# Performance work log

Measured on AMD Instinct MI355X. Metric: run time of the kernel, lower is better.

## Reference

```python
import jax, jax.numpy as jnp
import numpy as np

N_EMBD = 1024
N_HEAD = 16
HEAD_DIM = N_EMBD // N_HEAD


def setup_inputs() -> dict:
    key = jax.random.key(0)
    ks = jax.random.split(key, 9)
    B, T, C = 4, 2048, N_EMBD
    s = 1.0 / np.sqrt(C)
    return {
        "x": jax.random.normal(ks[0], (B, T, C), dtype=jnp.float32),
        "Wq": jax.random.normal(ks[1], (C, C), dtype=jnp.float32) * s,
        "bq": jnp.zeros((C,), dtype=jnp.float32),
        "Wk": jax.random.normal(ks[2], (C, C), dtype=jnp.float32) * s,
        "bk": jnp.zeros((C,), dtype=jnp.float32),
        "Wv": jax.random.normal(ks[3], (C, C), dtype=jnp.float32) * s,
        "bv": jnp.zeros((C,), dtype=jnp.float32),
        "Wo": jax.random.normal(ks[4], (C, C), dtype=jnp.float32) * s,
        "bo": jnp.zeros((C,), dtype=jnp.float32),
    }


def reference(x, Wq, bq, Wk, bk, Wv, bv, Wo, bo):
    B, T, C = x.shape
    H, D = N_HEAD, HEAD_DIM
    # torch Linear: y = x @ W.T + b ; here W stored as (in, out) so y = x @ W + b
    q = (x @ Wq + bq).reshape(B, T, H, D).transpose(0, 2, 1, 3)  # [B,H,T,D]
    k = (x @ Wk + bk).reshape(B, T, H, D).transpose(0, 2, 1, 3)
    v = (x @ Wv + bv).reshape(B, T, H, D).transpose(0, 2, 1, 3)
    scores = jnp.einsum('bhqd,bhkd->bhqk', q, k) / jnp.sqrt(jnp.float32(D))
    causal = jnp.tril(jnp.ones((T, T), dtype=bool))  # [T,T]
    scores = jnp.where(causal[None, None, :, :], scores, -jnp.inf)
    weights = jax.nn.softmax(scores, axis=-1)
    # dropout disabled (eval mode / deterministic reference)
    out = jnp.einsum('bhqk,bhkd->bhqd', weights, v)  # [B,H,T,D]
    out = out.transpose(0, 2, 1, 3).reshape(B, T, C)
    return out @ Wo + bo
```

## Files before the change

### kernel.cpp

```cpp
#include <hip/hip_runtime.h>
#include <stdint.h>
#include <stddef.h>

#define NB 4
#define NT 2048
#define NC 1024
#define NH 16
#define ND 64
#define NM (NB*NT)

typedef __bf16 bf16_t;
typedef __attribute__((ext_vector_type(8)))  __bf16 bf16x8;
typedef __attribute__((ext_vector_type(4)))  __bf16 bf16x4;
typedef __attribute__((ext_vector_type(2)))  __bf16 bf16x2;
typedef __attribute__((ext_vector_type(4)))  float  f32x4;
typedef __attribute__((ext_vector_type(16))) float  f32x16;
typedef __attribute__((ext_vector_type(4)))  unsigned int u32x4;

#define QK_SCALE_LOG2E 0.18033688011112042f

__device__ __forceinline__ f32x4 mfma_bf16(bf16x8 a, bf16x8 b, f32x4 c) {
  return __builtin_amdgcn_mfma_f32_16x16x32_bf16(a, b, c, 0, 0, 0);
}
__device__ __forceinline__ f32x16 mfma32(bf16x8 a, bf16x8 b, f32x16 c) {
  return __builtin_amdgcn_mfma_f32_32x32x16_bf16(a, b, c, 0, 0, 0);
}

__device__ __forceinline__ void gld_lds16(const void* g, void* l) {
  __builtin_amdgcn_global_load_lds(
      (const __attribute__((address_space(1))) void*)g,
      (__attribute__((address_space(3))) void*)l, 16, 0, 0);
}

__device__ __forceinline__ unsigned int pack_bf16(float a, float b) {
  bf16x2 t; t[0] = (bf16_t)a; t[1] = (bf16_t)b;
  return __builtin_bit_cast(unsigned int, t);
}

#if __has_builtin(__builtin_amdgcn_permlane32_swap)
typedef __attribute__((ext_vector_type(2))) unsigned int u32x2;
__device__ __forceinline__ void plswap(unsigned int &a, unsigned int &b) {
  u32x2 r = __builtin_amdgcn_permlane32_swap(a, b, false, false);
  a = r[0]; b = r[1];
}
#else
__device__ __forceinline__ void plswap(unsigned int &a, unsigned int &b) {
  asm volatile("s_nop 1\n\tv_permlane32_swap_b32 %0, %1\n\ts_nop 1"
               : "+v"(a), "+v"(b));
}
#endif

__global__ __launch_bounds__(256) void cast_x_kernel(const float* __restrict__ x,
                                                     bf16_t* __restrict__ xb, int n4) {
  const int stride = gridDim.x * blockDim.x;
  for (int i = blockIdx.x * blockDim.x + threadIdx.x; i < n4; i += stride) {
    float4 v = reinterpret_cast<const float4*>(x)[i];
    bf16x4 o;
    o[0] = (bf16_t)v.x; o[1] = (bf16_t)v.y; o[2] = (bf16_t)v.z; o[3] = (bf16_t)v.w;
    reinterpret_cast<bf16x4*>(xb)[i] = o;
  }
}

__global__ __launch_bounds__(256) void wtrans_kernel(
    const float* __restrict__ Wq, const float* __restrict__ Wk,
    const float* __restrict__ Wv, const float* __restrict__ Wo,
    bf16_t* __restrict__ Tq, bf16_t* __restrict__ Tk,
    bf16_t* __restrict__ Tv, bf16_t* __restrict__ To) {
  __shared__ float tile[32][33];
  const int wsel = blockIdx.x >> 10;
  const float* W = (wsel == 0) ? Wq : (wsel == 1) ? Wk : (wsel == 2) ? Wv : Wo;
  bf16_t*     WT = (wsel == 0) ? Tq : (wsel == 1) ? Tk : (wsel == 2) ? Tv : To;
  const int blk = blockIdx.x & 1023;
  const int t = threadIdx.x;
  const int tx = t & 31, ty = t >> 5;
  const int k0 = (blk & 31) << 5;
  const int n0 = (blk >> 5) << 5;
#pragma unroll
  for (int i = 0; i < 4; ++i)
    tile[ty + 8*i][tx] = W[(size_t)(k0 + ty + 8*i)*NC + n0 + tx];
  __syncthreads();
#pragma unroll
  for (int i = 0; i < 4; ++i)
    WT[(size_t)(n0 + ty + 8*i)*NC + k0 + tx] = (bf16_t)tile[tx][ty + 8*i];
}

__global__ __launch_bounds__(256) void vtrans_kernel(const bf16_t* __restrict__ v,
                                                     bf16_t* __restrict__ vt) {
  __shared__ bf16_t tile[64][72];
  const int tid = threadIdx.x;
  const int bh = blockIdx.x >> 5;
  const int t0 = (blockIdx.x & 31) << 6;
  const size_t base = (size_t)bh * (NT * ND);
  {
    const int r = tid >> 2, dc = (tid & 3) << 4;
    const bf16_t* src = v + base + (size_t)(t0 + r)*ND + dc;
    const bf16x8 a = *reinterpret_cast<const bf16x8*>(src);
    const bf16x8 b = *reinterpret_cast<const bf16x8*>(src + 8);
    *reinterpret_cast<bf16x8*>(&tile[r][dc])     = a;
    *reinterpret_cast<bf16x8*>(&tile[r][dc + 8]) = b;
  }
  __syncthreads();
  {
    const int d = tid >> 2, tc = (tid & 3) << 4;
    bf16x8 a, b;
#pragma unroll
    for (int i = 0; i < 8; ++i) { a[i] = tile[tc + i][d]; b[i] = tile[tc + 8 + i][d]; }
    bf16_t* dst = vt + base + (size_t)d*NT + t0 + tc;
    *reinterpret_cast<bf16x8*>(dst)     = a;
    *reinterpret_cast<bf16x8*>(dst + 8) = b;
  }
}

template<int MODE>
__global__ __launch_bounds__(512, 2) void gemm_bt256_kernel(
    const bf16_t* __restrict__ A, const bf16_t* __restrict__ BT,
    int M, int N, int K,
    bf16_t* __restrict__ qo, bf16_t* __restrict__ ko, bf16_t* __restrict__ vo,
    const float* __restrict__ b0, const float* __restrict__ b1, const float* __restrict__ b2,
    float* __restrict__ outp, const float* __restrict__ bo)
{
  const int tid  = threadIdx.x;
  const int lane = tid & 63;
  const int wv   = tid >> 6;
  const int wr   = wv >> 1, wc = wv & 1;
  const int l15  = lane & 15, lg = lane >> 4;

  const int nbn = N >> 7;
  const int cpx = gridDim.x >> 3;
  const int swz = (blockIdx.x & 7)*cpx + (blockIdx.x >> 3);
  const int bm = swz / nbn, bn = swz % nbn;
  const int m0 = bm << 8, n0 = bn << 7;

  __shared__ char smem[98304];

  f32x4 acc[4][4] = {};

  int offa[4], offb[2];
#pragma unroll
  for (int p = 0; p < 4; ++p) {
    const int c = p*512 + tid;
    const int row = c >> 3, ch = (c & 7) ^ (row & 7);
    offa[p] = row*K + (ch << 3);
  }
#pragma unroll
  for (int p = 0; p < 2; ++p) {
    const int c = p*512 + tid;
    const int row = c >> 3, ch = (c & 7) ^ (row & 7);
    offb[p] = row*K + (ch << 3);
  }
  const int sega = wv << 10;

  const bf16_t* Ab = A  + (size_t)m0 * K;
  const bf16_t* Bb = BT + (size_t)n0 * K;

  const int nkt = K >> 6;

  {
    char* const As = smem;
    char* const Bs = smem + 32768;
#pragma unroll
    for (int p = 0; p < 4; ++p) gld_lds16(Ab + offa[p], As + p*8192 + sega);
#pragma unroll
    for (int p = 0; p < 2; ++p) gld_lds16(Bb + offb[p], Bs + p*8192 + sega);
  }

  for (int kt = 0; kt < nkt; ++kt) {
    char* const As = smem + (kt & 1)*49152;
    char* const Bs = As + 32768;

    asm volatile("s_waitcnt vmcnt(0)" ::: "memory");
    __builtin_amdgcn_s_barrier();
    __builtin_amdgcn_sched_barrier(0);

    if (kt + 1 < nkt) {
      char* const An = smem + ((kt + 1) & 1)*49152;
      char* const Bn = An + 32768;
      const int k0 = (kt + 1) << 6;
#pragma unroll
      for (int p = 0; p < 4; ++p) gld_lds16(Ab + k0 + offa[p], An + p*8192 + sega);
#pragma unroll
      for (int p = 0; p < 2; ++p) gld_lds16(Bb + k0 + offb[p], Bn + p*8192 + sega);
      __builtin_amdgcn_sched_barrier(0);
    }

#pragma unroll
    for (int ks = 0; ks < 2; ++ks) {
      bf16x8 af[4], bfr[4];
#pragma unroll
      for (int fr = 0; fr < 4; ++fr) {
        const int row = wr*64 + fr*16 + l15;
        const int ch  = (ks*4 + lg) ^ (row & 7);
        af[fr] = *reinterpret_cast<const bf16x8*>(As + row*128 + ch*16);
      }
#pragma unroll
      for (int fc = 0; fc < 4; ++fc) {
        const int row = wc*64 + fc*16 + l15;
        const int ch  = (ks*4 + lg) ^ (row & 7);
        bfr[fc] = *reinterpret_cast<const bf16x8*>(Bs + row*128 + ch*16);
      }
      __builtin_amdgcn_s_setprio(1);
#pragma unroll
      for (int fr = 0; fr < 4; ++fr)
#pragma unroll
        for (int fc = 0; fc < 4; ++fc)
          acc[fr][fc] = mfma_bf16(af[fr], bfr[fc], acc[fr][fc]);
      __builtin_amdgcn_s_setprio(0);
    }
  }

#pragma unroll
  for (int fr = 0; fr < 4; ++fr) {
#pragma unroll
    for (int fc = 0; fc < 4; ++fc) {
      const int mrow0 = m0 + wr*64 + fr*16 + (lg << 2);
      const int ncol  = n0 + wc*64 + fc*16 + l15;
      if (MODE == 0) {
        const int mat = ncol >> 10, c = ncol & 1023;
        const int h = c >> 6, d = c & 63;
        bf16_t* dst = (mat == 0) ? qo : ((mat == 1) ? ko : vo);
        const float* bptr = (mat == 0) ? b0 : ((mat == 1) ? b1 : b2);
        const float bias = bptr[c];
        const float scl = (mat == 0) ? QK_SCALE_LOG2E : 1.0f;
#pragma unroll
        for (int r = 0; r < 4; ++r) {
          const int mm = mrow0 + r;
          const int bb = mm >> 11, tt = mm & (NT - 1);
          dst[((((size_t)bb*NH + h)*NT + tt) << 6) + d] =
              (bf16_t)((acc[fr][fc][r] + bias) * scl);
        }
      } else {
        const float bias = bo[ncol];
#pragma unroll
        for (int r = 0; r < 4; ++r)
          outp[(size_t)(mrow0 + r)*N + ncol] = acc[fr][fc][r] + bias;
      }
    }
  }
}

__global__ __launch_bounds__(256, 2) void attn_kernel(
    const bf16_t* __restrict__ q, const bf16_t* __restrict__ k, const bf16_t* __restrict__ vt,
    bf16_t* __restrict__ o)
{
  const int tid  = threadIdx.x;
  const int lane = tid & 63;
  const int wv   = tid >> 6;
  const int l31  = lane & 31, h = lane >> 5;

  const int tpair = blockIdx.x >> 6;
  const int bh    = blockIdx.x & 63;
  const int bb = bh >> 4, hh = bh & 15;

  __shared__ char smem[65536];
  char* const ks0 = smem;
  char* const ks1 = smem + 16384;
  char* const vs0 = smem + 32768;
  char* const vs1 = smem + 49152;

  const size_t base = (size_t)bh * (NT * ND);
  const bf16_t* Kg = k  + base;
  const bf16_t* Vg = vt + base;

  int offk[4], offv[4], segb[4];
#pragma unroll
  for (int p = 0; p < 4; ++p) {
    const int c = p*256 + tid;
    const int krow = c >> 3;
    const int kch  = (c & 7) ^ (krow & 7);
    offk[p] = krow*ND + (kch << 3);
    const int vrow = c >> 4;
    const int vdc  = (c & 15) ^ (vrow & 15);
    offv[p] = vrow*NT + (vdc << 3);
    segb[p] = (p*4 + wv) << 10;
  }

  bf16x8 ones8;
#pragma unroll
  for (int jj2 = 0; jj2 < 8; ++jj2) ones8[jj2] = (bf16_t)1.0f;

#pragma unroll
  for (int p = 0; p < 4; ++p) {
    gld_lds16(Kg + offk[p], ks0 + segb[p]);
    gld_lds16(Vg + offv[p], vs0 + segb[p]);
  }

  int jj = 0;

#pragma unroll 1
  for (int pass = 0; pass < 2; ++pass) {
    const int tile = (pass == 0) ? tpair : 15 - tpair;
    const int q0   = tile << 7;
    const int q0w  = q0 + wv*32;
    const int qg   = q0w + l31;

    bf16x8 qf[4];
    {
      const bf16_t* Qg = q + base + (size_t)qg*ND + 8*h;
#pragma unroll
      for (int ds = 0; ds < 4; ++ds)
        qf[ds] = *reinterpret_cast<const bf16x8*>(Qg + 16*ds);
    }

    f32x16 oc[2] = {};
    f32x16 lacc = {};

    const int nkv = tile + 1;

#pragma unroll 1
    for (int j = 0; j < nkv; ++j, ++jj) {
      const bool cur1 = (jj & 1) != 0;
      char* const Kc = cur1 ? ks1 : ks0;
      char* const Vc = cur1 ? vs1 : vs0;

      asm volatile("s_waitcnt vmcnt(0)" ::: "memory");
      __builtin_amdgcn_s_barrier();
      __builtin_amdgcn_sched_barrier(0);

      int nj = (j + 1 < nkv) ? (j + 1) : ((pass == 0) ? 0 : -1);
      if (nj >= 0) {
        char* const Kn = cur1 ? ks0 : ks1;
        char* const Vn = cur1 ? vs0 : vs1;
        const bf16_t* kp = Kg + (size_t)nj*(128*ND);
        const bf16_t* vp = Vg + (size_t)nj*128;
#pragma unroll
        for (int p = 0; p < 4; ++p) {
          gld_lds16(kp + offk[p], Kn + segb[p]);
          gld_lds16(vp + offv[p], Vn + segb[p]);
        }
        __builtin_amdgcn_sched_barrier(0);
      }

      const int ktile0 = j << 7;
#pragma unroll 1
      for (int hf = 0; hf < 2; ++hf) {
        const int kb0 = ktile0 + (hf << 6);
        if (kb0 > q0w + 31) break;

        f32x16 st[2] = {};
        __builtin_amdgcn_s_setprio(1);
#pragma unroll
        for (int ds = 0; ds < 4; ++ds) {
#pragma unroll
          for (int kt = 0; kt < 2; ++kt) {
            const int row = (hf*2 + kt)*32 + l31;
            const int cl  = (2*ds + h) ^ (row & 7);
            const bf16x8 kfr = *reinterpret_cast<const bf16x8*>(Kc + row*128 + cl*16);
            st[kt] = mfma32(kfr, qf[ds], st[kt]);
          }
        }
        __builtin_amdgcn_s_setprio(0);

        if (kb0 + 63 > q0w) {
          const int qrel = qg - kb0 - 4*h;
#pragma unroll
          for (int kt = 0; kt < 2; ++kt)
#pragma unroll
            for (int r = 0; r < 16; ++r) {
              const int kc = (r & 3) + 8*(r >> 2) + 32*kt;
              st[kt][r] = (kc > qrel) ? 0.0f : exp2f(st[kt][r]);
            }
        } else {
#pragma unroll
          for (int kt = 0; kt < 2; ++kt)
#pragma unroll
            for (int r = 0; r < 16; ++r)
              st[kt][r] = exp2f(st[kt][r]);
        }

#pragma unroll
        for (int kt = 0; kt < 2; ++kt) {
#pragma unroll
          for (int g = 0; g < 2; ++g) {
            unsigned int wa = pack_bf16(st[kt][8*g + 0], st[kt][8*g + 1]);
            unsigned int wb = pack_bf16(st[kt][8*g + 2], st[kt][8*g + 3]);
            unsigned int wc = pack_bf16(st[kt][8*g + 4], st[kt][8*g + 5]);
            unsigned int wd = pack_bf16(st[kt][8*g + 6], st[kt][8*g + 7]);
            plswap(wa, wc);
            plswap(wb, wd);
            u32x4 pb; pb[0] = wa; pb[1] = wb; pb[2] = wc; pb[3] = wd;
            const bf16x8 pf = __builtin_bit_cast(bf16x8, pb);
            const int cv = 2*(4*hf + 2*kt + g) + h;
            __builtin_amdgcn_s_setprio(1);
            lacc = mfma32(ones8, pf, lacc);
#pragma unroll
            for (int da = 0; da < 2; ++da) {
              const int row = 32*da + l31;
              const int lcv = cv ^ (row & 15);
              const bf16x8 vf = *reinterpret_cast<const bf16x8*>(Vc + row*256 + lcv*16);
              oc[da] = mfma32(vf, pf, oc[da]);
            }
            __builtin_amdgcn_s_setprio(0);
          }
        }
      }
    }

    const float rl = 1.0f / lacc[0];
    bf16_t* orow = o + ((size_t)bb*NT + qg)*NC + hh*ND;
#pragma unroll
    for (int da = 0; da < 2; ++da) {
#pragma unroll
      for (int u = 0; u < 4; ++u) {
        bf16x4 ov;
#pragma unroll
        for (int jj3 = 0; jj3 < 4; ++jj3) ov[jj3] = (bf16_t)(oc[da][4*u + jj3] * rl);
        *reinterpret_cast<bf16x4*>(orow + 32*da + 8*u + 4*h) = ov;
      }
    }
  }
}

extern "C" void kernel_launch(void* const* d_in, const int* in_sizes, int n_in,
                              void* d_out, int out_size, void* d_ws, size_t ws_size,
                              hipStream_t stream) {
  (void)in_sizes; (void)n_in; (void)out_size;
  const float* x  = (const float*)d_in[0];
  const float* Wq = (const float*)d_in[1];
  const float* bq = (const float*)d_in[2];
  const float* Wk = (const float*)d_in[3];
  const float* bk = (const float*)d_in[4];
  const float* Wv = (const float*)d_in[5];
  const float* bv = (const float*)d_in[6];
  const float* Wo = (const float*)d_in[7];
  const float* bo = (const float*)d_in[8];
  float* out = (float*)d_out;

  const size_t off_xb    = 0;
  const size_t off_wqkvT = 16777216;
  const size_t off_woT   = 23068672;
  const size_t off_q     = 25165824;
  const size_t off_k     = 41943040;
  const size_t off_v     = 58720256;
  const size_t off_attn  = 75497472;
  const size_t need      = 92274688;
  if (ws_size < need) return;

  char* ws = (char*)d_ws;
  bf16_t* xb    = (bf16_t*)(ws + off_xb);
  bf16_t* wqkvT = (bf16_t*)(ws + off_wqkvT);
  bf16_t* woT   = (bf16_t*)(ws + off_woT);
  bf16_t* qb    = (bf16_t*)(ws + off_q);
  bf16_t* kb    = (bf16_t*)(ws + off_k);
  bf16_t* vb    = (bf16_t*)(ws + off_v);
  bf16_t* vtb   = (bf16_t*)(ws + off_xb);
  bf16_t* attnb = (bf16_t*)(ws + off_attn);

  cast_x_kernel<<<dim3(2048), dim3(256), 0, stream>>>(x, xb, NM*NC/4);
  wtrans_kernel<<<dim3(4096), dim3(256), 0, stream>>>(
      Wq, Wk, Wv, Wo, wqkvT, wqkvT + 1048576, wqkvT + 2097152, woT);

  gemm_bt256_kernel<0><<<dim3(768), dim3(512), 0, stream>>>(
      xb, wqkvT, NM, 3*NC, NC, qb, kb, vb, bq, bk, bv, nullptr, nullptr);

  vtrans_kernel<<<dim3(2048), dim3(256), 0, stream>>>(vb, vtb);

  attn_kernel<<<dim3(8*64), dim3(256), 0, stream>>>(qb, kb, vtb, attnb);

  gemm_bt256_kernel<1><<<dim3(256), dim3(512), 0, stream>>>(
      attnb, woT, NM, NC, NC, nullptr, nullptr, nullptr, nullptr, nullptr, nullptr,
      out, bo);
}
```

Before: 168.7 us.

## Fuse V transpose into QKV GEMM epilogue and merge prep kernels

The QKV GEMM epilogue for V-column tiles now stages results in shared memory and writes V directly in transposed [b,h,d,t] layout with vectorized stores. This removes the separate vtrans kernel launch and its extra read and write of V. The x cast and weight transpose kernels are also merged into one launch. The cost is an extra LDS round trip and two barriers in the V-tile epilogue, and a branchy combined prep kernel.

```diff
diff --git a/kernel.cpp b/kernel.cpp
--- a/kernel.cpp
+++ b/kernel.cpp
@@ -50,64 +50,38 @@
 }
 #endif
 
-__global__ __launch_bounds__(256) void cast_x_kernel(const float* __restrict__ x,
-                                                     bf16_t* __restrict__ xb, int n4) {
-  const int stride = gridDim.x * blockDim.x;
-  for (int i = blockIdx.x * blockDim.x + threadIdx.x; i < n4; i += stride) {
-    float4 v = reinterpret_cast<const float4*>(x)[i];
-    bf16x4 o;
-    o[0] = (bf16_t)v.x; o[1] = (bf16_t)v.y; o[2] = (bf16_t)v.z; o[3] = (bf16_t)v.w;
-    reinterpret_cast<bf16x4*>(xb)[i] = o;
-  }
-}
-
-__global__ __launch_bounds__(256) void wtrans_kernel(
-    const float* __restrict__ Wq, const float* __restrict__ Wk,
-    const float* __restrict__ Wv, const float* __restrict__ Wo,
-    bf16_t* __restrict__ Tq, bf16_t* __restrict__ Tk,
+__global__ __launch_bounds__(256) void prep_kernel(
+    const float* __restrict__ x, const float* __restrict__ Wq,
+    const float* __restrict__ Wk, const float* __restrict__ Wv,
+    const float* __restrict__ Wo,
+    bf16_t* __restrict__ xb, bf16_t* __restrict__ Tq, bf16_t* __restrict__ Tk,
     bf16_t* __restrict__ Tv, bf16_t* __restrict__ To) {
   __shared__ float tile[32][33];
-  const int wsel = blockIdx.x >> 10;
-  const float* W = (wsel == 0) ? Wq : (wsel == 1) ? Wk : (wsel == 2) ? Wv : Wo;
-  bf16_t*     WT = (wsel == 0) ? Tq : (wsel == 1) ? Tk : (wsel == 2) ? Tv : To;
-  const int blk = blockIdx.x & 1023;
-  const int t = threadIdx.x;
-  const int tx = t & 31, ty = t >> 5;
-  const int k0 = (blk & 31) << 5;
-  const int n0 = (blk >> 5) << 5;
-#pragma unroll
-  for (int i = 0; i < 4; ++i)
-    tile[ty + 8*i][tx] = W[(size_t)(k0 + ty + 8*i)*NC + n0 + tx];
-  __syncthreads();
-#pragma unroll
-  for (int i = 0; i < 4; ++i)
-    WT[(size_t)(n0 + ty + 8*i)*NC + k0 + tx] = (bf16_t)tile[tx][ty + 8*i];
-}
-
-__global__ __launch_bounds__(256) void vtrans_kernel(const bf16_t* __restrict__ v,
-                                                     bf16_t* __restrict__ vt) {
-  __shared__ bf16_t tile[64][72];
-  const int tid = threadIdx.x;
-  const int bh = blockIdx.x >> 5;
-  const int t0 = (blockIdx.x & 31) << 6;
-  const size_t base = (size_t)bh * (NT * ND);
-  {
-    const int r = tid >> 2, dc = (tid & 3) << 4;
-    const bf16_t* src = v + base + (size_t)(t0 + r)*ND + dc;
-    const bf16x8 a = *reinterpret_cast<const bf16x8*>(src);
-    const bf16x8 b = *reinterpret_cast<const bf16x8*>(src + 8);
-    *reinterpret_cast<bf16x8*>(&tile[r][dc])     = a;
-    *reinterpret_cast<bf16x8*>(&tile[r][dc + 8]) = b;
-  }
-  __syncthreads();
-  {
-    const int d = tid >> 2, tc = (tid & 3) << 4;
-    bf16x8 a, b;
-#pragma unroll
-    for (int i = 0; i < 8; ++i) { a[i] = tile[tc + i][d]; b[i] = tile[tc + 8 + i][d]; }
-    bf16_t* dst = vt + base + (size_t)d*NT + t0 + tc;
-    *reinterpret_cast<bf16x8*>(dst)     = a;
-    *reinterpret_cast<bf16x8*>(dst + 8) = b;
+  if (blockIdx.x < 4096) {
+    const int wsel = blockIdx.x >> 10;
+    const float* W = (wsel == 0) ? Wq : (wsel == 1) ? Wk : (wsel == 2) ? Wv : Wo;
+    bf16_t*     WT = (wsel == 0) ? Tq : (wsel == 1) ? Tk : (wsel == 2) ? Tv : To;
+    const int blk = blockIdx.x & 1023;
+    const int t = threadIdx.x;
+    const int tx = t & 31, ty = t >> 5;
+    const int k0 = (blk & 31) << 5;
+    const int n0 = (blk >> 5) << 5;
+#pragma unroll
+    for (int i = 0; i < 4; ++i)
+      tile[ty + 8*i][tx] = W[(size_t)(k0 + ty + 8*i)*NC + n0 + tx];
+    __syncthreads();
+#pragma unroll
+    for (int i = 0; i < 4; ++i)
+      WT[(size_t)(n0 + ty + 8*i)*NC + k0 + tx] = (bf16_t)tile[tx][ty + 8*i];
+  } else {
+    const int n4 = NM*NC/4;
+    const int stride = 2048 * 256;
+    for (int i = (blockIdx.x - 4096) * 256 + threadIdx.x; i < n4; i += stride) {
+      float4 v = reinterpret_cast<const float4*>(x)[i];
+      bf16x4 o;
+      o[0] = (bf16_t)v.x; o[1] = (bf16_t)v.y; o[2] = (bf16_t)v.z; o[3] = (bf16_t)v.w;
+      reinterpret_cast<bf16x4*>(xb)[i] = o;
+    }
   }
 }
 
@@ -208,31 +182,61 @@
     }
   }
 
-#pragma unroll
-  for (int fr = 0; fr < 4; ++fr) {
-#pragma unroll
-    for (int fc = 0; fc < 4; ++fc) {
-      const int mrow0 = m0 + wr*64 + fr*16 + (lg << 2);
-      const int ncol  = n0 + wc*64 + fc*16 + l15;
-      if (MODE == 0) {
-        const int mat = ncol >> 10, c = ncol & 1023;
-        const int h = c >> 6, d = c & 63;
-        bf16_t* dst = (mat == 0) ? qo : ((mat == 1) ? ko : vo);
-        const float* bptr = (mat == 0) ? b0 : ((mat == 1) ? b1 : b2);
-        const float bias = bptr[c];
-        const float scl = (mat == 0) ? QK_SCALE_LOG2E : 1.0f;
-#pragma unroll
-        for (int r = 0; r < 4; ++r) {
-          const int mm = mrow0 + r;
-          const int bb = mm >> 11, tt = mm & (NT - 1);
-          dst[((((size_t)bb*NH + h)*NT + tt) << 6) + d] =
-              (bf16_t)((acc[fr][fc][r] + bias) * scl);
+  if (MODE == 0 && n0 >= 2*NC) {
+    bf16_t* vbuf = (bf16_t*)smem;
+    const int VSTR = 264;
+    __syncthreads();
+#pragma unroll
+    for (int fr = 0; fr < 4; ++fr) {
+#pragma unroll
+      for (int fc = 0; fc < 4; ++fc) {
+        const int zl = wc*64 + fc*16 + l15;
+        const int tl = wr*64 + fr*16 + (lg << 2);
+        const float bias = b2[(n0 - 2*NC) + zl];
+        bf16x4 ov;
+#pragma unroll
+        for (int r = 0; r < 4; ++r) ov[r] = (bf16_t)(acc[fr][fc][r] + bias);
+        *reinterpret_cast<bf16x4*>(&vbuf[zl*VSTR + tl]) = ov;
+      }
+    }
+    __syncthreads();
+    const int zl  = tid >> 2;
+    const int t0l = (tid & 3) << 6;
+    const int zg  = (n0 - 2*NC) + zl;
+    const int h   = zg >> 6, d = zg & 63;
+    const int bbv = m0 >> 11;
+    bf16_t* dst = vo + ((((size_t)bbv*NH + h)*ND + d)*NT) + (m0 & (NT-1)) + t0l;
+#pragma unroll
+    for (int u = 0; u < 8; ++u)
+      *reinterpret_cast<bf16x8*>(dst + u*8) =
+          *reinterpret_cast<const bf16x8*>(&vbuf[zl*VSTR + t0l + u*8]);
+  } else {
+#pragma unroll
+    for (int fr = 0; fr < 4; ++fr) {
+#pragma unroll
+      for (int fc = 0; fc < 4; ++fc) {
+        const int mrow0 = m0 + wr*64 + fr*16 + (lg << 2);
+        const int ncol  = n0 + wc*64 + fc*16 + l15;
+        if (MODE == 0) {
+          const int mat = ncol >> 10, c = ncol & 1023;
+          const int h = c >> 6, d = c & 63;
+          bf16_t* dst = (mat == 0) ? qo : ko;
+          const float* bptr = (mat == 0) ? b0 : b1;
+          const float bias = bptr[c];
+          const float scl = (mat == 0) ? QK_SCALE_LOG2E : 1.0f;
+#pragma unroll
+          for (int r = 0; r < 4; ++r) {
+            const int mm = mrow0 + r;
+            const int bb = mm >> 11, tt = mm & (NT - 1);
+            dst[((((size_t)bb*NH + h)*NT + tt) << 6) + d] =
+                (bf16_t)((acc[fr][fc][r] + bias) * scl);
+          }
+        } else {
+          const float bias = bo[ncol];
+#pragma unroll
+          for (int r = 0; r < 4; ++r)
+            outp[(size_t)(mrow0 + r)*N + ncol] = acc[fr][fc][r] + bias;
         }
-      } else {
-        const float bias = bo[ncol];
-#pragma unroll
-        for (int r = 0; r < 4; ++r)
-          outp[(size_t)(mrow0 + r)*N + ncol] = acc[fr][fc][r] + bias;
       }
     }
   }
@@ -441,18 +445,14 @@
   bf16_t* woT   = (bf16_t*)(ws + off_woT);
   bf16_t* qb    = (bf16_t*)(ws + off_q);
   bf16_t* kb    = (bf16_t*)(ws + off_k);
-  bf16_t* vb    = (bf16_t*)(ws + off_v);
-  bf16_t* vtb   = (bf16_t*)(ws + off_xb);
+  bf16_t* vtb   = (bf16_t*)(ws + off_v);
   bf16_t* attnb = (bf16_t*)(ws + off_attn);
 
-  cast_x_kernel<<<dim3(2048), dim3(256), 0, stream>>>(x, xb, NM*NC/4);
-  wtrans_kernel<<<dim3(4096), dim3(256), 0, stream>>>(
-      Wq, Wk, Wv, Wo, wqkvT, wqkvT + 1048576, wqkvT + 2097152, woT);
+  prep_kernel<<<dim3(6144), dim3(256), 0, stream>>>(
+      x, Wq, Wk, Wv, Wo, xb, wqkvT, wqkvT + 1048576, wqkvT + 2097152, woT);
 
   gemm_bt256_kernel<0><<<dim3(768), dim3(512), 0, stream>>>(
-      xb, wqkvT, NM, 3*NC, NC, qb, kb, vb, bq, bk, bv, nullptr, nullptr);
-
-  vtrans_kernel<<<dim3(2048), dim3(256), 0, stream>>>(vb, vtb);
+      xb, wqkvT, NM, 3*NC, NC, qb, kb, vtb, bq, bk, bv, nullptr, nullptr);
 
   attn_kernel<<<dim3(8*64), dim3(256), 0, stream>>>(qb, kb, vtb, attnb);
 
```

Measured after the change: 161.3 us. -4.3%, faster.
